# Optimization experiments

Hardware: AMD Instinct MI355X
Metric: run time of the kernel (lower is better)

## Reference

```python
import jax, jax.numpy as jnp
import numpy as np
import math

H, W, K = 512, 512, 16
B = 64


def _U(r2):
    # torch: r**2 * log(r**2 + 1e-6), with r = euclidean norm -> r2 = squared norm
    return r2 * jnp.log(r2 + 1e-6)


def _base_control_points():
    k_sqrt = int(math.sqrt(K))
    x = jnp.linspace(-1.0, 1.0, k_sqrt)
    y = jnp.linspace(-1.0, 1.0, k_sqrt)
    gx, gy = jnp.meshgrid(x, y, indexing='ij')  # torch default meshgrid is 'ij'
    return jnp.stack([gx.ravel(), gy.ravel()], axis=1)  # [K, 2]


def _target_grid():
    x = jnp.linspace(-1.0, 1.0, W)
    y = jnp.linspace(-1.0, 1.0, H)
    gy, gx = jnp.meshgrid(y, x, indexing='ij')
    return jnp.stack([gx.ravel(), gy.ravel()], axis=1)  # [H*W, 2]


def setup_inputs() -> dict:
    key = jax.random.key(0)
    source_points = jax.random.normal(key, (B, K, 2), dtype=jnp.float32)
    return {"source_points": source_points}


def reference(source_points):
    cp = _base_control_points()      # [K, 2]
    grid = _target_grid()            # [HW, 2]

    # Delta matrix (K+3, K+3). Diagonal of U-block is 0 (matches i != j loop since U(0)=0).
    d = cp[:, None, :] - cp[None, :, :]
    r2 = jnp.sum(d * d, axis=-1)
    Ukk = _U(r2)
    delta = jnp.zeros((K + 3, K + 3), dtype=source_points.dtype)
    delta = delta.at[:K, :K].set(Ukk)
    delta = delta.at[:K, K].set(1.0)
    delta = delta.at[:K, K + 1:].set(cp)
    delta = delta.at[K, :K].set(1.0)
    delta = delta.at[K + 1:, :K].set(cp.T)
    inv_delta = jnp.linalg.inv(delta)  # computed once, shared across batch

    # Batched coefficients: param matrix = [source_points ; zeros(3,2)]
    Pm = jnp.concatenate(
        [source_points, jnp.zeros((source_points.shape[0], 3, 2), dtype=source_points.dtype)],
        axis=1,
    )  # [B, K+3, 2]
    coeff = jnp.einsum('ij,bjd->bid', inv_delta, Pm)  # [B, K+3, 2]

    # RBF basis for target grid (batch-independent): [HW, K]
    dg = grid[:, None, :] - cp[None, :, :]
    Ug = _U(jnp.sum(dg * dg, axis=-1))
    # Affine part: [1, x, y]
    Pg = jnp.concatenate([jnp.ones((grid.shape[0], 1), dtype=grid.dtype), grid], axis=1)  # [HW, 3]

    out = jnp.einsum('nk,bkd->bnd', Ug, coeff[:, :K, :]) + jnp.einsum('nt,btd->bnd', Pg, coeff[:, K:, :])
    return out.reshape(source_points.shape[0], H, W, 2)
```

## Files before the change

kernel.cpp:

```cpp
#include <hip/hip_runtime.h>

#define HH 512
#define WW 512
#define KK 16
#define BB 64
#define HW (HH*WW)

constexpr double cx_ln(double x) {
  int e = 0;
  while (x >= 2.0) { x *= 0.5; ++e; }
  while (x < 1.0)  { x *= 2.0; --e; }
  double z = (x - 1.0) / (x + 1.0);
  double z2 = z * z, term = z, sum = 0.0;
  for (int n = 1; n < 60; n += 2) { sum += term / n; term *= z2; }
  return 2.0 * sum + e * 0.69314718055994530942;
}

struct WMat { float w[19][16]; };

constexpr WMat build_wm() {
  const double Xc[4] = {-1.0, -1.0/3.0, 1.0/3.0, 1.0};
  double A[19][38] = {};
  for (int r = 0; r < 19; ++r) {
    for (int c = 0; c < 38; ++c) {
      double v = 0.0;
      if (c >= 19) {
        v = ((c - 19) == r) ? 1.0 : 0.0;
      } else if (r < 16 && c < 16) {
        double dx = Xc[r >> 2] - Xc[c >> 2];
        double dy = Xc[r & 3] - Xc[c & 3];
        double r2 = dx * dx + dy * dy;
        v = (r2 == 0.0) ? 0.0 : r2 * cx_ln(r2 + 1e-6);
      } else if (r < 16) {
        v = (c == 16) ? 1.0 : ((c == 17) ? Xc[r >> 2] : Xc[r & 3]);
      } else if (c < 16) {
        v = (r == 16) ? 1.0 : ((r == 17) ? Xc[c >> 2] : Xc[c & 3]);
      }
      A[r][c] = v;
    }
  }
  for (int k = 0; k < 19; ++k) {
    int best = k;
    double bv = A[k][k] < 0 ? -A[k][k] : A[k][k];
    for (int r = k + 1; r < 19; ++r) {
      double av = A[r][k] < 0 ? -A[r][k] : A[r][k];
      if (av > bv) { bv = av; best = r; }
    }
    if (best != k)
      for (int c = 0; c < 38; ++c) { double t = A[k][c]; A[k][c] = A[best][c]; A[best][c] = t; }
    double rp = 1.0 / A[k][k];
    for (int c = 0; c < 38; ++c) A[k][c] *= rp;
    for (int r = 0; r < 19; ++r) {
      if (r == k) continue;
      double f = A[r][k];
      for (int c = 0; c < 38; ++c) A[r][c] -= f * A[k][c];
    }
  }
  WMat wm = {};
  for (int i = 0; i < 19; ++i)
    for (int j = 0; j < 16; ++j)
      wm.w[i][j] = (float)(A[i][19 + j] * (i < 16 ? 0.69314718055994530942 : 1.0));
  return wm;
}

__device__ __constant__ WMat WM = build_wm();

__global__ __launch_bounds__(256) void tps_grid_kernel(
    const float* __restrict__ sp, float* __restrict__ out) {
  __shared__ float cs[40];
  const int tid = threadIdx.x;
  const int b = blockIdx.y;

  if (tid < 38) {
    const int i = tid >> 1, d = tid & 1;
    const float* s = sp + b * 32 + d;
    float acc = 0.0f;
#pragma unroll
    for (int j = 0; j < 16; ++j) acc = fmaf(WM.w[i][j], s[2 * j], acc);
    cs[tid] = acc;
  }
  __syncthreads();

  float cc[38];
#pragma unroll
  for (int i = 0; i < 9; ++i) {
    float4 t = ((const float4*)cs)[i];
    cc[4 * i] = t.x; cc[4 * i + 1] = t.y; cc[4 * i + 2] = t.z; cc[4 * i + 3] = t.w;
  }
  cc[36] = cs[36]; cc[37] = cs[37];

  const int n0 = (blockIdx.x * 256 + tid) * 4;
  const int ix = n0 & (WW - 1);
  const int iy = n0 >> 9;
  const float step = 2.0f / 511.0f;
  const float gy = -1.0f + iy * step;
  const float Xc[4] = {-1.0f, -1.0f / 3.0f, 1.0f / 3.0f, 1.0f};

  float dy2[4];
#pragma unroll
  for (int j = 0; j < 4; ++j) { float t = gy - Xc[j]; dy2[j] = t * t; }

  float gx[4], dx2[4][4];
#pragma unroll
  for (int p = 0; p < 4; ++p) {
    gx[p] = -1.0f + (ix + p) * step;
#pragma unroll
    for (int i = 0; i < 4; ++i) {
      float t = gx[p] - Xc[i];
      dx2[p][i] = fmaf(t, t, 1e-6f);
    }
  }

  float ax[4], ay[4];
#pragma unroll
  for (int p = 0; p < 4; ++p) {
    ax[p] = cc[32] + gx[p] * cc[34] + gy * cc[36];
    ay[p] = cc[33] + gx[p] * cc[35] + gy * cc[37];
  }

#pragma unroll
  for (int k = 0; k < 16; ++k) {
    const float wx = cc[2 * k], wy = cc[2 * k + 1];
#pragma unroll
    for (int p = 0; p < 4; ++p) {
      float t = dx2[p][k >> 2] + dy2[k & 3];
      float u = t * __log2f(t);
      ax[p] = fmaf(u, wx, ax[p]);
      ay[p] = fmaf(u, wy, ay[p]);
    }
  }

  float* o = out + (size_t)(b * HW + n0) * 2;
  *(float4*)o       = make_float4(ax[0], ay[0], ax[1], ay[1]);
  *((float4*)o + 1) = make_float4(ax[2], ay[2], ax[3], ay[3]);
}

extern "C" void kernel_launch(void* const* d_in, const int* in_sizes, int n_in,
                              void* d_out, int out_size, void* d_ws, size_t ws_size,
                              hipStream_t stream) {
  const float* sp = (const float*)d_in[0];
  float* out = (float*)d_out;

  dim3 grid(HW / 1024, BB);
  tps_grid_kernel<<<grid, 256, 0, stream>>>(sp, out);
}
```

Measured before the change: 150.0 us.

## Split coefficient solve into its own kernel and reuse RBF basis across batches

A small first kernel now computes the per-batch TPS coefficients into workspace. The grid kernel computes the log-based RBF basis once per pixel pair and reuses it for a group of 16 batches, which removes the transcendental work repeated per batch. It also uses packed float2 arithmetic and nontemporal stores. In exchange it adds a second launch, a workspace dependency, per-batch coefficient reloads from global memory, and fewer blocks in the grid.

```diff
diff --git a/kernel.cpp b/kernel.cpp
--- a/kernel.cpp
+++ b/kernel.cpp
@@ -2,9 +2,13 @@
 
 #define HH 512
 #define WW 512
-#define KK 16
 #define BB 64
 #define HW (HH*WW)
+#define CSTRIDE 40
+#define BGRP 16
+
+typedef float v2f __attribute__((ext_vector_type(2)));
+typedef float v4f __attribute__((ext_vector_type(4)));
 
 constexpr double cx_ln(double x) {
   int e = 0;
@@ -65,74 +69,75 @@
 
 __device__ __constant__ WMat WM = build_wm();
 
-__global__ __launch_bounds__(256) void tps_grid_kernel(
-    const float* __restrict__ sp, float* __restrict__ out) {
-  __shared__ float cs[40];
+__device__ __forceinline__ float fast_log2(float x) {
+#if __has_builtin(__builtin_amdgcn_logf)
+  return __builtin_amdgcn_logf(x);
+#else
+  return __log2f(x);
+#endif
+}
+
+__global__ __launch_bounds__(64) void tps_coeff_kernel(
+    const float* __restrict__ sp, float* __restrict__ coeff) {
+  const int b = blockIdx.x;
   const int tid = threadIdx.x;
-  const int b = blockIdx.y;
-
   if (tid < 38) {
     const int i = tid >> 1, d = tid & 1;
     const float* s = sp + b * 32 + d;
     float acc = 0.0f;
 #pragma unroll
     for (int j = 0; j < 16; ++j) acc = fmaf(WM.w[i][j], s[2 * j], acc);
-    cs[tid] = acc;
+    coeff[b * CSTRIDE + tid] = acc;
   }
-  __syncthreads();
+}
 
-  float cc[38];
-#pragma unroll
-  for (int i = 0; i < 9; ++i) {
-    float4 t = ((const float4*)cs)[i];
-    cc[4 * i] = t.x; cc[4 * i + 1] = t.y; cc[4 * i + 2] = t.z; cc[4 * i + 3] = t.w;
-  }
-  cc[36] = cs[36]; cc[37] = cs[37];
-
-  const int n0 = (blockIdx.x * 256 + tid) * 4;
+__global__ __launch_bounds__(256) void tps_grid_kernel(
+    const float* __restrict__ coeff, float* __restrict__ out) {
+  const int n0 = (blockIdx.x * 256 + threadIdx.x) * 2;
   const int ix = n0 & (WW - 1);
   const int iy = n0 >> 9;
   const float step = 2.0f / 511.0f;
   const float gy = -1.0f + iy * step;
+  const v2f gxv = {-1.0f + ix * step, -1.0f + (ix + 1) * step};
   const float Xc[4] = {-1.0f, -1.0f / 3.0f, 1.0f / 3.0f, 1.0f};
 
   float dy2[4];
 #pragma unroll
   for (int j = 0; j < 4; ++j) { float t = gy - Xc[j]; dy2[j] = t * t; }
 
-  float gx[4], dx2[4][4];
+  v2f dxp[4];
 #pragma unroll
-  for (int p = 0; p < 4; ++p) {
-    gx[p] = -1.0f + (ix + p) * step;
-#pragma unroll
-    for (int i = 0; i < 4; ++i) {
-      float t = gx[p] - Xc[i];
-      dx2[p][i] = fmaf(t, t, 1e-6f);
-    }
+  for (int i = 0; i < 4; ++i) {
+    v2f t = gxv - Xc[i];
+    dxp[i] = t * t + 1e-6f;
   }
 
-  float ax[4], ay[4];
+  v2f u2[16];
 #pragma unroll
-  for (int p = 0; p < 4; ++p) {
-    ax[p] = cc[32] + gx[p] * cc[34] + gy * cc[36];
-    ay[p] = cc[33] + gx[p] * cc[35] + gy * cc[37];
+  for (int k = 0; k < 16; ++k) {
+    v2f t = dxp[k >> 2] + dy2[k & 3];
+    u2[k] = t * (v2f){fast_log2(t.x), fast_log2(t.y)};
   }
 
+  const int b0 = blockIdx.y * BGRP;
+  for (int bi = 0; bi < BGRP; ++bi) {
+    const int b = b0 + bi;
+    const float* __restrict__ c = coeff + b * CSTRIDE;
+    float cc[38];
 #pragma unroll
-  for (int k = 0; k < 16; ++k) {
-    const float wx = cc[2 * k], wy = cc[2 * k + 1];
+    for (int i = 0; i < 38; ++i) cc[i] = c[i];
+
+    v2f accx = cc[32] + gxv * cc[34] + gy * cc[36];
+    v2f accy = cc[33] + gxv * cc[35] + gy * cc[37];
 #pragma unroll
-    for (int p = 0; p < 4; ++p) {
-      float t = dx2[p][k >> 2] + dy2[k & 3];
-      float u = t * __log2f(t);
-      ax[p] = fmaf(u, wx, ax[p]);
-      ay[p] = fmaf(u, wy, ay[p]);
+    for (int k = 0; k < 16; ++k) {
+      accx += u2[k] * cc[2 * k];
+      accy += u2[k] * cc[2 * k + 1];
     }
+
+    v4f v = {accx.x, accy.x, accx.y, accy.y};
+    __builtin_nontemporal_store(v, (v4f*)(out + (size_t)(b * HW + n0) * 2));
   }
-
-  float* o = out + (size_t)(b * HW + n0) * 2;
-  *(float4*)o       = make_float4(ax[0], ay[0], ax[1], ay[1]);
-  *((float4*)o + 1) = make_float4(ax[2], ay[2], ax[3], ay[3]);
 }
 
 extern "C" void kernel_launch(void* const* d_in, const int* in_sizes, int n_in,
@@ -140,7 +145,10 @@
                               hipStream_t stream) {
   const float* sp = (const float*)d_in[0];
   float* out = (float*)d_out;
+  float* coeff = (float*)d_ws;
 
-  dim3 grid(HW / 1024, BB);
-  tps_grid_kernel<<<grid, 256, 0, stream>>>(sp, out);
+  tps_coeff_kernel<<<BB, 64, 0, stream>>>(sp, coeff);
+
+  dim3 grid(HW / 512, BB / BGRP);
+  tps_grid_kernel<<<grid, 256, 0, stream>>>(coeff, out);
 }
```

New measurement: 140.7 us. 6.2% less time.
